# Performance work log

Hardware: AMD Instinct MI355X
Metric: run time of the kernel (lower is better)

The kernel has to match this reference:

```python
import jax, jax.numpy as jnp
import numpy as np

B, S, DM, DE, H, DH, DC, DCq, DR = 4, 2048, 1024, 1024, 16, 64, 128, 128, 32
SCALE = 1.0 / np.sqrt(DH + DR)


def _rope_tables(seq_len, dim, theta=10000.0):
    inv = 1.0 / (theta ** (jnp.arange(0, dim, 2, dtype=jnp.float32) / dim))  # [dim/2]
    t = jnp.arange(seq_len, dtype=jnp.float32)
    ang = t[:, None] * inv[None, :]  # [S, dim/2]
    return jnp.cos(ang), jnp.sin(ang)


def _apply_rope(xq, xk, cos, sin):
    # xq, xk: [B, S, H, DR]; complex rotary on (even, odd) pairs
    def rot(x):
        s = x.shape
        xr = x.reshape(*s[:-1], s[-1] // 2, 2)
        r, i = xr[..., 0], xr[..., 1]
        c = cos[None, :s[1], None, :]
        sn = sin[None, :s[1], None, :]
        out = jnp.stack([r * c - i * sn, r * sn + i * c], axis=-1)
        return out.reshape(s)
    return rot(xq), rot(xk)


def setup_inputs() -> dict:
    key = jax.random.key(0)
    ks = jax.random.split(key, 10)
    def lin(k, din, dout):
        return 0.02 * jax.random.normal(k, (din, dout), jnp.float32)
    inp = {
        "x": jax.random.normal(ks[0], (B, S, DM), jnp.float32),
        "mask": jnp.tril(jnp.ones((S, S), jnp.float32))[None, None],
        "W_dkv": lin(ks[1], DM, DC),  "b_dkv": jnp.zeros((DC,), jnp.float32),
        "W_dq":  lin(ks[2], DM, DCq), "b_dq":  jnp.zeros((DCq,), jnp.float32),
        "W_uk":  lin(ks[3], DC, DE),  "b_uk":  jnp.zeros((DE,), jnp.float32),
        "W_uv":  lin(ks[4], DC, DE),  "b_uv":  jnp.zeros((DE,), jnp.float32),
        "W_uq":  lin(ks[5], DCq, DE), "b_uq":  jnp.zeros((DE,), jnp.float32),
        "W_qr":  lin(ks[6], DCq, DR * H), "b_qr": jnp.zeros((DR * H,), jnp.float32),
        "W_kr":  lin(ks[7], DM, DR),  "b_kr": jnp.zeros((DR,), jnp.float32),
        "W_o":   lin(ks[8], DE, DM),  "b_o":  jnp.zeros((DM,), jnp.float32),
    }
    return inp


def reference(x, mask, W_dkv, b_dkv, W_dq, b_dq, W_uk, b_uk, W_uv, b_uv,
              W_uq, b_uq, W_qr, b_qr, W_kr, b_kr, W_o, b_o):
    bs, seq_len, _ = x.shape
    cos, sin = _rope_tables(2 * S, DR)

    c_q = x @ W_dq + b_dq            # [B,S,DCq]
    c_kv = x @ W_dkv + b_dkv         # [B,S,DC]
    k_r = x @ W_kr + b_kr            # [B,S,DR]

    q_c = (c_q @ W_uq + b_uq).reshape(bs, seq_len, H, DH)
    k_c = (c_kv @ W_uk + b_uk).reshape(bs, seq_len, H, DH)
    v_c = (c_kv @ W_uv + b_uv).reshape(bs, seq_len, H, DH)

    q_r = (c_q @ W_qr + b_qr).reshape(bs, seq_len, H, DR)
    k_r = jnp.broadcast_to(k_r[:, :, None, :], (bs, seq_len, H, DR))
    q_r, k_r = _apply_rope(q_r, k_r, cos, sin)

    q_t = jnp.concatenate([q_c, q_r], axis=-1)  # [B,S,H,DH+DR]
    k_t = jnp.concatenate([k_c, k_r], axis=-1)

    attn = jnp.einsum('bqhd,bkhd->bhqk', q_t, k_t) * SCALE  # [B,H,S,S]
    m = jnp.where(mask == 0, -jnp.inf, mask)  # faithful masked_fill then add
    attn = attn + m
    p = jax.nn.softmax(attn, axis=-1)
    out = jnp.einsum('bhqk,bkhd->bqhd', p, v_c).reshape(bs, seq_len, H * DH)
    return out @ W_o + b_o
```

## Files before the change

### kernel.cpp

```cpp
#include <hip/hip_runtime.h>
#include <cstdint>
#include <cstddef>

#define S_ 2048
#define B_ 4
#define H_ 16
#define ALPHA_Q 0.14724394f

typedef __attribute__((ext_vector_type(8))) __bf16 bf16x8;
typedef __attribute__((ext_vector_type(4))) __bf16 bf16x4;
typedef __attribute__((ext_vector_type(4))) float f32x4;
typedef __attribute__((ext_vector_type(16))) float f32x16;

__device__ __forceinline__ f32x16 mfma32(bf16x8 a, bf16x8 b, f32x16 c) {
  return __builtin_amdgcn_mfma_f32_32x32x16_bf16(a, b, c, 0, 0, 0);
}

__device__ __forceinline__ void gll16(const void* g, void* l) {
  __builtin_amdgcn_global_load_lds(
      (__attribute__((address_space(1))) void*)(uintptr_t)g,
      (__attribute__((address_space(3))) void*)(uint32_t)(uintptr_t)l,
      16, 0, 0);
}

__device__ __forceinline__ int cvtpk(float lo, float hi) {
  int r;
  asm("v_cvt_pk_bf16_f32 %0, %1, %2" : "=v"(r) : "v"(lo), "v"(hi));
  return r;
}

union PAU { int w[4]; bf16x8 v; };

__device__ __forceinline__ bf16x8 packPA(int hi, float a0, float a1, float a2,
                                         float a3, float b0, float b1, float b2,
                                         float b3) {
  const int Ylo = cvtpk(a0, a1);
  const int Yhi = cvtpk(a2, a3);
  const int Xlo = cvtpk(b0, b1);
  const int Xhi = cvtpk(b2, b3);
  const int t0 = __shfl_xor(hi ? Ylo : Xlo, 32);
  const int t1 = __shfl_xor(hi ? Yhi : Xhi, 32);
  PAU u;
  u.w[0] = hi ? t0 : Ylo;
  u.w[1] = hi ? t1 : Yhi;
  u.w[2] = hi ? Xlo : t0;
  u.w[3] = hi ? Xhi : t1;
  return u.v;
}


__global__ __launch_bounds__(256) void mla_cvt_x(const float* __restrict__ x,
                                                 __bf16* __restrict__ xb) {
  const size_t i = ((size_t)blockIdx.x * 256 + threadIdx.x) * 8;
  float4 a = *(const float4*)&x[i];
  float4 b = *(const float4*)&x[i + 4];
  bf16x8 v;
  v[0] = (__bf16)a.x; v[1] = (__bf16)a.y; v[2] = (__bf16)a.z; v[3] = (__bf16)a.w;
  v[4] = (__bf16)b.x; v[5] = (__bf16)b.y; v[6] = (__bf16)b.z; v[7] = (__bf16)b.w;
  *(bf16x8*)&xb[i] = v;
}

__global__ void mla_transpose(const float* __restrict__ W, __bf16* __restrict__ WT,
                              int K, int N) {
  __shared__ float tile[32][33];
  const int n0 = blockIdx.x * 32, k0 = blockIdx.y * 32;
  const int tx = threadIdx.x, ty = threadIdx.y;
#pragma unroll
  for (int i = 0; i < 32; i += 8)
    tile[ty + i][tx] = W[(size_t)(k0 + ty + i) * N + n0 + tx];
  __syncthreads();
#pragma unroll
  for (int i = 0; i < 32; i += 8)
    WT[(size_t)(n0 + ty + i) * K + k0 + tx] = (__bf16)tile[tx][ty + i];
}

__global__ void mla_bias(const float* __restrict__ b_dq, const float* __restrict__ b_dkv,
                         const float* __restrict__ b_kr, const float* __restrict__ b_uq,
                         const float* __restrict__ b_qr, const float* __restrict__ b_uk,
                         const float* __restrict__ b_uv, float* __restrict__ bias_d,
                         float* __restrict__ bias_uq, float* __restrict__ bias_ukv) {
  const int t = blockIdx.x * 256 + threadIdx.x;
  if (t < 384)
    bias_d[t] = (t < 128) ? b_dq[t] : (t < 256) ? b_dkv[t - 128]
               : (t < 288) ? b_kr[t - 256] : 0.f;
  if (t < 1536) bias_uq[t] = (t < 1024) ? b_uq[t] : b_qr[t - 1024];
  if (t < 2048) bias_ukv[t] = (t < 1024) ? b_uk[t] : b_uv[t - 1024];
}

__global__ void mla_rope_tab(float* __restrict__ c, float* __restrict__ sn) {
  const int t = blockIdx.x * 256 + threadIdx.x;
  const int s = t >> 4, i = t & 15;
  const float inv = exp2f(-(float)i * (13.287712379549449f / 16.0f));
  const float ang = (float)s * inv;
  c[t] = cosf(ang);
  sn[t] = sinf(ang);
}

template <int MODE>
__global__ __launch_bounds__(256) void gemm32(
    const __bf16* __restrict__ A, int lda, const __bf16* __restrict__ BT, int ldbt,
    const float* __restrict__ bias, void* __restrict__ C0, void* __restrict__ C1,
    int ldc, int K) {
  const int n0 = blockIdx.x * 128;
  const int m0 = blockIdx.y * 128;
  const int wave = threadIdx.x >> 6, lane = threadIdx.x & 63;
  const int hi = lane >> 5, lq = lane & 31;
  const int wm = (wave >> 1) * 64, wn = (wave & 1) * 64;
  __shared__ __bf16 __attribute__((aligned(16))) ldsA[8 * 128 * 8];
  __shared__ __bf16 __attribute__((aligned(16))) ldsB[8 * 128 * 8];

  const f32x16 fz16 = {0.f, 0.f, 0.f, 0.f, 0.f, 0.f, 0.f, 0.f,
                       0.f, 0.f, 0.f, 0.f, 0.f, 0.f, 0.f, 0.f};
  f32x16 acc00 = fz16, acc01 = fz16, acc10 = fz16, acc11 = fz16;

  for (int k0 = 0; k0 < K; k0 += 64) {
    __syncthreads();
#pragma unroll
    for (int i = 0; i < 8; ++i) {
      const int c = wave * 8 + i;
      if (c < 16) {
        const int sl = c >> 1, half = c & 1;
        gll16(&A[(size_t)(m0 + half * 64 + lane) * lda + k0 + sl * 8],
              &ldsA[(sl * 128 + half * 64) * 8]);
      } else {
        const int cc = c - 16;
        const int sl = cc >> 1, half = cc & 1;
        gll16(&BT[(size_t)(n0 + half * 64 + lane) * ldbt + k0 + sl * 8],
              &ldsB[(sl * 128 + half * 64) * 8]);
      }
    }
    __syncthreads();

#pragma unroll
    for (int ks = 0; ks < 4; ++ks) {
      const int sl = ks * 2 + hi;
      bf16x8 a0 = *(const bf16x8*)&ldsA[(sl * 128 + wm + lq) * 8];
      bf16x8 a1 = *(const bf16x8*)&ldsA[(sl * 128 + wm + 32 + lq) * 8];
      bf16x8 b0 = *(const bf16x8*)&ldsB[(sl * 128 + wn + lq) * 8];
      bf16x8 b1 = *(const bf16x8*)&ldsB[(sl * 128 + wn + 32 + lq) * 8];
      acc00 = mfma32(a0, b0, acc00);
      acc01 = mfma32(a0, b1, acc01);
      acc10 = mfma32(a1, b0, acc10);
      acc11 = mfma32(a1, b1, acc11);
    }
  }

  const f32x16* accs[2][2] = {{&acc00, &acc01}, {&acc10, &acc11}};
#pragma unroll
  for (int ni = 0; ni < 2; ++ni) {
    const int col = n0 + wn + ni * 32 + lq;
    const float bv = bias[col];
#pragma unroll
    for (int mi = 0; mi < 2; ++mi) {
      const f32x16& ac = *accs[mi][ni];
#pragma unroll
      for (int r = 0; r < 16; ++r) {
        const int row = m0 + wm + mi * 32 + (r & 3) + 8 * (r >> 2) + 4 * hi;
        const float v = ac[r] + bv;
        if (MODE == 0) {
          ((__bf16*)C0)[(size_t)row * ldc + col] = (__bf16)v;
        } else if (MODE == 1) {
          ((float*)C0)[(size_t)row * ldc + col] = v;
        } else {
          const int b = row >> 11, s = row & 2047;
          if (col < 1024) {
            const int h = col >> 6, d = col & 63;
            const size_t o = ((size_t)(b * H_ + h) * S_ + s) * 96 + d;
            if (MODE == 2)
              ((__bf16*)C0)[o] = (__bf16)(v * ALPHA_Q);
            else
              ((__bf16*)C0)[o] = (__bf16)v;
          } else {
            if (MODE == 2)
              ((__bf16*)C1)[(size_t)row * 512 + col - 1024] = (__bf16)v;
            else
              ((__bf16*)C1)[(size_t)row * 1024 + col - 1024] = (__bf16)v;
          }
        }
      }
    }
  }
}

__global__ __launch_bounds__(256) void mla_rope_qk(
    const __bf16* __restrict__ qr, const __bf16* __restrict__ cqkvr,
    const float* __restrict__ ropec, const float* __restrict__ ropes,
    __bf16* __restrict__ qt, __bf16* __restrict__ ktb) {
  const int gid = blockIdx.x * 256 + threadIdx.x;
  const int bs = gid >> 8;
  const int h = (gid >> 4) & 15;
  const int i = gid & 15;
  const int b = bs >> 11, s = bs & 2047;
  const float c = ropec[s * 16 + i], sn = ropes[s * 16 + i];
  const size_t o = ((size_t)(b * H_ + h) * S_ + s) * 96 + 64 + 2 * i;
  {
    const float r = (float)qr[(size_t)bs * 512 + h * 32 + 2 * i];
    const float im = (float)qr[(size_t)bs * 512 + h * 32 + 2 * i + 1];
    qt[o] = (__bf16)((r * c - im * sn) * ALPHA_Q);
    qt[o + 1] = (__bf16)((r * sn + im * c) * ALPHA_Q);
  }
  {
    const float r = (float)cqkvr[(size_t)bs * 384 + 256 + 2 * i];
    const float im = (float)cqkvr[(size_t)bs * 384 + 256 + 2 * i + 1];
    ktb[o] = (__bf16)(r * c - im * sn);
    ktb[o + 1] = (__bf16)(r * sn + im * c);
  }
}

__global__ __launch_bounds__(256) void mla_vtrans(const __bf16* __restrict__ vv,
                                                  __bf16* __restrict__ vt) {
  const int s0 = blockIdx.x * 64;
  const int bh = blockIdx.y;
  const int b = bh >> 4, h = bh & 15;
  __shared__ __bf16 __attribute__((aligned(16))) tile[64][72];
  const int t = threadIdx.x;
  {
    const int r = t >> 2, c0 = (t & 3) * 16;
    const size_t src = (size_t)(b * S_ + s0 + r) * 1024 + h * 64 + c0;
    bf16x8 u0 = *(const bf16x8*)&vv[src];
    bf16x8 u1 = *(const bf16x8*)&vv[src + 8];
    *(bf16x8*)&tile[r][c0] = u0;
    *(bf16x8*)&tile[r][c0 + 8] = u1;
  }
  __syncthreads();
  {
    const int d = t >> 2, sc0 = (t & 3) * 16;
    bf16x8 w0, w1;
#pragma unroll
    for (int e = 0; e < 8; ++e) {
      w0[e] = tile[sc0 + e][d];
      w1[e] = tile[sc0 + 8 + e][d];
    }
    const size_t dst = ((size_t)bh * 64 + d) * S_ + s0 + sc0;
    *(bf16x8*)&vt[dst] = w0;
    *(bf16x8*)&vt[dst + 8] = w1;
  }
}

__global__ __launch_bounds__(256, 3) void mla_attn(const __bf16* __restrict__ qt,
                                                   const __bf16* __restrict__ kt,
                                                   const __bf16* __restrict__ vt,
                                                   __bf16* __restrict__ ao) {
  const int qblk = (int)gridDim.x - 1 - blockIdx.x;
  const int bh = blockIdx.y;
  const int wave = threadIdx.x >> 6, lane = threadIdx.x & 63;
  const int hi = lane >> 5, lq = lane & 31;
  const int q0w = qblk * 128 + wave * 32;
  const __bf16* Q = qt + (size_t)bh * S_ * 96;
  const __bf16* Kp = kt + (size_t)bh * S_ * 96;
  const __bf16* Vp = vt + (size_t)bh * 64 * S_;

  __shared__ __bf16 __attribute__((aligned(16))) kbuf[2][12 * 512];
  __shared__ __bf16 __attribute__((aligned(16))) vbuf[2][8 * 512];

  bf16x8 qf[6];
#pragma unroll
  for (int kd = 0; kd < 6; ++kd)
    qf[kd] = *(const bf16x8*)&Q[(size_t)(q0w + lq) * 96 + kd * 16 + hi * 8];

  const f32x16 fz16 = {0.f, 0.f, 0.f, 0.f, 0.f, 0.f, 0.f, 0.f,
                       0.f, 0.f, 0.f, 0.f, 0.f, 0.f, 0.f, 0.f};
  f32x16 o0 = fz16, o1 = fz16;
  float m = -3.0e38f, L = 0.f;

  const int tEnd = (q0w + 31) >> 6;
  const int tMax = qblk * 2 + 1;

  auto stage = [&](int t, int bsel) {
    const int kv0 = t * 64;
#pragma unroll
    for (int i = 0; i < 5; ++i) {
      const int c = wave + 4 * i;
      if (c < 12)
        gll16(&Kp[(size_t)(kv0 + lane) * 96 + c * 8], &kbuf[bsel][c * 512]);
      else
        gll16(&Vp[(size_t)lane * S_ + kv0 + (c - 12) * 8], &vbuf[bsel][(c - 12) * 512]);
    }
  };

  stage(0, 0);
  __syncthreads();

  int bsel = 0;
  for (int t = 0; t <= tMax; ++t) {
    if (t < tMax) stage(t + 1, bsel ^ 1);
    if (t <= tEnd) {
      f32x16 s0 = fz16, s1 = fz16;
#pragma unroll
      for (int kd = 0; kd < 6; ++kd) {
        const int sl = kd * 2 + hi;
        bf16x8 a0 = *(const bf16x8*)&kbuf[bsel][(sl * 64 + lq) * 8];
        bf16x8 a1 = *(const bf16x8*)&kbuf[bsel][(sl * 64 + 32 + lq) * 8];
        s0 = mfma32(a0, qf[kd], s0);
        s1 = mfma32(a1, qf[kd], s1);
      }
      if (t == tEnd) {
        const int qg = q0w + lq;
        const int kvb = t * 64 + 4 * hi;
#pragma unroll
        for (int r = 0; r < 16; ++r) {
          const int crow = (r & 3) + 8 * (r >> 2);
          if (kvb + crow > qg) s0[r] = -3.0e38f;
          if (kvb + 32 + crow > qg) s1[r] = -3.0e38f;
        }
      }
      float tm = s0[0];
#pragma unroll
      for (int r = 1; r < 16; ++r) tm = fmaxf(tm, s0[r]);
#pragma unroll
      for (int r = 0; r < 16; ++r) tm = fmaxf(tm, s1[r]);
      tm = fmaxf(tm, __shfl_xor(tm, 32));
      const float mnew = fmaxf(m, tm);
      float p0[16], p1[16];
      float ps = 0.f;
#pragma unroll
      for (int r = 0; r < 16; ++r) {
        p0[r] = exp2f(s0[r] - mnew);
        p1[r] = exp2f(s1[r] - mnew);
        ps += p0[r] + p1[r];
      }
      ps += __shfl_xor(ps, 32);
      const float sc = exp2f(m - mnew);
      L = L * sc + ps;
      m = mnew;
      o0 *= sc;
      o1 *= sc;
      bf16x8 pa[4];
      pa[0] = packPA(hi, p0[0], p0[1], p0[2], p0[3], p0[4], p0[5], p0[6], p0[7]);
      pa[1] = packPA(hi, p0[8], p0[9], p0[10], p0[11], p0[12], p0[13], p0[14], p0[15]);
      pa[2] = packPA(hi, p1[0], p1[1], p1[2], p1[3], p1[4], p1[5], p1[6], p1[7]);
      pa[3] = packPA(hi, p1[8], p1[9], p1[10], p1[11], p1[12], p1[13], p1[14], p1[15]);
#pragma unroll
      for (int ks = 0; ks < 4; ++ks) {
        const int sl = ks * 2 + hi;
        bf16x8 v0 = *(const bf16x8*)&vbuf[bsel][(sl * 64 + lq) * 8];
        bf16x8 v1 = *(const bf16x8*)&vbuf[bsel][(sl * 64 + 32 + lq) * 8];
        o0 = mfma32(v0, pa[ks], o0);
        o1 = mfma32(v1, pa[ks], o1);
      }
    }
    __syncthreads();
    bsel ^= 1;
  }

  const float invL = 1.0f / L;
  const int bb = bh >> 4, h = bh & 15;
  __bf16* aorow = ao + (size_t)(bb * S_ + q0w + lq) * 1024 + h * 64;
#pragma unroll
  for (int rr = 0; rr < 4; ++rr) {
    bf16x4 w0, w1;
#pragma unroll
    for (int j = 0; j < 4; ++j) {
      w0[j] = (__bf16)(o0[4 * rr + j] * invL);
      w1[j] = (__bf16)(o1[4 * rr + j] * invL);
    }
    *(bf16x4*)&aorow[rr * 8 + 4 * hi] = w0;
    *(bf16x4*)&aorow[32 + rr * 8 + 4 * hi] = w1;
  }
}

extern "C" void kernel_launch(void* const* d_in, const int* in_sizes, int n_in,
                              void* d_out, int out_size, void* d_ws, size_t ws_size,
                              hipStream_t stream) {
  (void)in_sizes; (void)n_in; (void)out_size; (void)ws_size;
  const float* x = (const float*)d_in[0];
  const float* W_dkv = (const float*)d_in[2];
  const float* b_dkv = (const float*)d_in[3];
  const float* W_dq = (const float*)d_in[4];
  const float* b_dq = (const float*)d_in[5];
  const float* W_uk = (const float*)d_in[6];
  const float* b_uk = (const float*)d_in[7];
  const float* W_uv = (const float*)d_in[8];
  const float* b_uv = (const float*)d_in[9];
  const float* W_uq = (const float*)d_in[10];
  const float* b_uq = (const float*)d_in[11];
  const float* W_qr = (const float*)d_in[12];
  const float* b_qr = (const float*)d_in[13];
  const float* W_kr = (const float*)d_in[14];
  const float* b_kr = (const float*)d_in[15];
  const float* W_o = (const float*)d_in[16];
  const float* b_o = (const float*)d_in[17];
  float* out = (float*)d_out;

  char* ws = (char*)d_ws;
  size_t off = 0;
  auto take = [&](size_t nbytes) -> char* {
    char* p = ws + off;
    off += (nbytes + 255) & ~(size_t)255;
    return p;
  };
  __bf16* xb = (__bf16*)take((size_t)8192 * 1024 * 2);
  __bf16* WdT = (__bf16*)take((size_t)384 * 1024 * 2);
  __bf16* WuqT = (__bf16*)take((size_t)1536 * 128 * 2);
  __bf16* WukvT = (__bf16*)take((size_t)2048 * 128 * 2);
  __bf16* WoT = (__bf16*)take((size_t)1024 * 1024 * 2);
  float* bias_d = (float*)take(384 * 4);
  float* bias_uq = (float*)take(1536 * 4);
  float* bias_ukv = (float*)take(2048 * 4);
  float* ropec = (float*)take((size_t)S_ * 16 * 4);
  float* ropes = (float*)take((size_t)S_ * 16 * 4);
  __bf16* cqkvr = (__bf16*)take((size_t)8192 * 384 * 2);
  __bf16* qr = (__bf16*)take((size_t)8192 * 512 * 2);
  __bf16* vv = (__bf16*)take((size_t)8192 * 1024 * 2);
  __bf16* qt = (__bf16*)take((size_t)B_ * H_ * S_ * 96 * 2);
  __bf16* ktb = (__bf16*)take((size_t)B_ * H_ * S_ * 96 * 2);
  __bf16* vt = (__bf16*)take((size_t)B_ * H_ * 64 * S_ * 2);
  __bf16* aout = (__bf16*)take((size_t)8192 * 1024 * 2);

  hipMemsetAsync(WdT + (size_t)288 * 1024, 0, (size_t)96 * 1024 * 2, stream);

  mla_cvt_x<<<4096, 256, 0, stream>>>(x, xb);
  mla_transpose<<<dim3(4, 32), dim3(32, 8), 0, stream>>>(W_dq, WdT, 1024, 128);
  mla_transpose<<<dim3(4, 32), dim3(32, 8), 0, stream>>>(W_dkv, WdT + (size_t)128 * 1024, 1024, 128);
  mla_transpose<<<dim3(1, 32), dim3(32, 8), 0, stream>>>(W_kr, WdT + (size_t)256 * 1024, 1024, 32);
  mla_transpose<<<dim3(32, 4), dim3(32, 8), 0, stream>>>(W_uq, WuqT, 128, 1024);
  mla_transpose<<<dim3(16, 4), dim3(32, 8), 0, stream>>>(W_qr, WuqT + (size_t)1024 * 128, 128, 512);
  mla_transpose<<<dim3(32, 4), dim3(32, 8), 0, stream>>>(W_uk, WukvT, 128, 1024);
  mla_transpose<<<dim3(32, 4), dim3(32, 8), 0, stream>>>(W_uv, WukvT + (size_t)1024 * 128, 128, 1024);
  mla_transpose<<<dim3(32, 32), dim3(32, 8), 0, stream>>>(W_o, WoT, 1024, 1024);
  mla_bias<<<8, 256, 0, stream>>>(b_dq, b_dkv, b_kr, b_uq, b_qr, b_uk, b_uv,
                                  bias_d, bias_uq, bias_ukv);
  mla_rope_tab<<<(S_ * 16) / 256, 256, 0, stream>>>(ropec, ropes);

  gemm32<0><<<dim3(3, 64), 256, 0, stream>>>(xb, 1024, WdT, 1024, bias_d,
                                             cqkvr, nullptr, 384, 1024);
  gemm32<2><<<dim3(12, 64), 256, 0, stream>>>(cqkvr, 384, WuqT, 128, bias_uq,
                                              qt, qr, 0, 128);
  gemm32<3><<<dim3(16, 64), 256, 0, stream>>>(cqkvr + 128, 384, WukvT, 128,
                                              bias_ukv, ktb, vv, 0, 128);

  mla_rope_qk<<<8192, 256, 0, stream>>>(qr, cqkvr, ropec, ropes, qt, ktb);
  mla_vtrans<<<dim3(32, 64), 256, 0, stream>>>(vv, vt);
  mla_attn<<<dim3(16, 64), 256, 0, stream>>>(qt, ktb, vt, aout);

  gemm32<1><<<dim3(8, 64), 256, 0, stream>>>(aout, 1024, WoT, 1024, b_o, out,
                                             nullptr, 1024, 1024);
}
```

Baseline: 412.4 us.

## Merge prep and glue kernels into single launches and use lazy softmax rescale

After: 388.3 us. 1.06x faster.

```diff
diff --git a/kernel.cpp b/kernel.cpp
--- a/kernel.cpp
+++ b/kernel.cpp
@@ -48,52 +48,86 @@
   return u.v;
 }
 
-
-__global__ __launch_bounds__(256) void mla_cvt_x(const float* __restrict__ x,
-                                                 __bf16* __restrict__ xb) {
-  const size_t i = ((size_t)blockIdx.x * 256 + threadIdx.x) * 8;
-  float4 a = *(const float4*)&x[i];
-  float4 b = *(const float4*)&x[i + 4];
-  bf16x8 v;
-  v[0] = (__bf16)a.x; v[1] = (__bf16)a.y; v[2] = (__bf16)a.z; v[3] = (__bf16)a.w;
-  v[4] = (__bf16)b.x; v[5] = (__bf16)b.y; v[6] = (__bf16)b.z; v[7] = (__bf16)b.w;
-  *(bf16x8*)&xb[i] = v;
-}
-
-__global__ void mla_transpose(const float* __restrict__ W, __bf16* __restrict__ WT,
-                              int K, int N) {
+__device__ __forceinline__ float tmax16(const f32x16& v) {
+  float a[8];
+#pragma unroll
+  for (int i = 0; i < 8; ++i) a[i] = fmaxf(v[i], v[i + 8]);
+#pragma unroll
+  for (int s = 4; s > 0; s >>= 1)
+#pragma unroll
+    for (int i = 0; i < s; ++i) a[i] = fmaxf(a[i], a[i + s]);
+  return a[0];
+}
+
+__global__ __launch_bounds__(256) void mla_prep(
+    const float* __restrict__ x, __bf16* __restrict__ xb,
+    const float* __restrict__ W_dq, const float* __restrict__ W_dkv,
+    const float* __restrict__ W_kr, const float* __restrict__ W_uq,
+    const float* __restrict__ W_qr, const float* __restrict__ W_uk,
+    const float* __restrict__ W_uv, const float* __restrict__ W_o,
+    __bf16* __restrict__ WdT, __bf16* __restrict__ WuqT,
+    __bf16* __restrict__ WukvT, __bf16* __restrict__ WoT,
+    const float* __restrict__ b_dq, const float* __restrict__ b_dkv,
+    const float* __restrict__ b_kr, const float* __restrict__ b_uq,
+    const float* __restrict__ b_qr, const float* __restrict__ b_uk,
+    const float* __restrict__ b_uv, float* __restrict__ bias_d,
+    float* __restrict__ bias_uq, float* __restrict__ bias_ukv,
+    float* __restrict__ ropec, float* __restrict__ ropes) {
+  const int id = blockIdx.x;
+  const int t = threadIdx.x;
   __shared__ float tile[32][33];
-  const int n0 = blockIdx.x * 32, k0 = blockIdx.y * 32;
-  const int tx = threadIdx.x, ty = threadIdx.y;
-#pragma unroll
-  for (int i = 0; i < 32; i += 8)
-    tile[ty + i][tx] = W[(size_t)(k0 + ty + i) * N + n0 + tx];
-  __syncthreads();
-#pragma unroll
-  for (int i = 0; i < 32; i += 8)
-    WT[(size_t)(n0 + ty + i) * K + k0 + tx] = (__bf16)tile[tx][ty + i];
-}
-
-__global__ void mla_bias(const float* __restrict__ b_dq, const float* __restrict__ b_dkv,
-                         const float* __restrict__ b_kr, const float* __restrict__ b_uq,
-                         const float* __restrict__ b_qr, const float* __restrict__ b_uk,
-                         const float* __restrict__ b_uv, float* __restrict__ bias_d,
-                         float* __restrict__ bias_uq, float* __restrict__ bias_ukv) {
-  const int t = blockIdx.x * 256 + threadIdx.x;
-  if (t < 384)
-    bias_d[t] = (t < 128) ? b_dq[t] : (t < 256) ? b_dkv[t - 128]
-               : (t < 288) ? b_kr[t - 256] : 0.f;
-  if (t < 1536) bias_uq[t] = (t < 1024) ? b_uq[t] : b_qr[t - 1024];
-  if (t < 2048) bias_ukv[t] = (t < 1024) ? b_uk[t] : b_uv[t - 1024];
-}
-
-__global__ void mla_rope_tab(float* __restrict__ c, float* __restrict__ sn) {
-  const int t = blockIdx.x * 256 + threadIdx.x;
-  const int s = t >> 4, i = t & 15;
-  const float inv = exp2f(-(float)i * (13.287712379549449f / 16.0f));
-  const float ang = (float)s * inv;
-  c[t] = cosf(ang);
-  sn[t] = sinf(ang);
+
+  if (id < 4096) {
+    const size_t i = ((size_t)id * 256 + t) * 8;
+    float4 a = *(const float4*)&x[i];
+    float4 b = *(const float4*)&x[i + 4];
+    bf16x8 v;
+    v[0] = (__bf16)a.x; v[1] = (__bf16)a.y; v[2] = (__bf16)a.z; v[3] = (__bf16)a.w;
+    v[4] = (__bf16)b.x; v[5] = (__bf16)b.y; v[6] = (__bf16)b.z; v[7] = (__bf16)b.w;
+    *(bf16x8*)&xb[i] = v;
+    return;
+  }
+  if (id < 5856) {
+    int rel = id - 4096;
+    const float* W;
+    __bf16* WT;
+    int K, N, nt;
+    if (rel < 128)      { W = W_dq;  WT = WdT;                      K = 1024; N = 128;  nt = 4; }
+    else if (rel < 256) { W = W_dkv; WT = WdT + (size_t)128 * 1024; K = 1024; N = 128;  nt = 4;  rel -= 128; }
+    else if (rel < 288) { W = W_kr;  WT = WdT + (size_t)256 * 1024; K = 1024; N = 32;   nt = 1;  rel -= 256; }
+    else if (rel < 416) { W = W_uq;  WT = WuqT;                     K = 128;  N = 1024; nt = 32; rel -= 288; }
+    else if (rel < 480) { W = W_qr;  WT = WuqT + (size_t)1024 * 128; K = 128; N = 512;  nt = 16; rel -= 416; }
+    else if (rel < 608) { W = W_uk;  WT = WukvT;                    K = 128;  N = 1024; nt = 32; rel -= 480; }
+    else if (rel < 736) { W = W_uv;  WT = WukvT + (size_t)1024 * 128; K = 128; N = 1024; nt = 32; rel -= 608; }
+    else                { W = W_o;   WT = WoT;                      K = 1024; N = 1024; nt = 32; rel -= 736; }
+    const int n0 = (rel % nt) * 32, k0 = (rel / nt) * 32;
+    const int tx = t & 31, ty = t >> 5;
+#pragma unroll
+    for (int i = 0; i < 32; i += 8)
+      tile[ty + i][tx] = W[(size_t)(k0 + ty + i) * N + n0 + tx];
+    __syncthreads();
+#pragma unroll
+    for (int i = 0; i < 32; i += 8)
+      WT[(size_t)(n0 + ty + i) * K + k0 + tx] = (__bf16)tile[tx][ty + i];
+    return;
+  }
+  if (id < 5984) {
+    const int g = (id - 5856) * 256 + t;
+    const int s = g >> 4, i = g & 15;
+    const float inv = exp2f(-(float)i * (13.287712379549449f / 16.0f));
+    const float ang = (float)s * inv;
+    ropec[g] = cosf(ang);
+    ropes[g] = sinf(ang);
+    return;
+  }
+  {
+    const int g = (id - 5984) * 256 + t;
+    if (g < 384)
+      bias_d[g] = (g < 128) ? b_dq[g] : (g < 256) ? b_dkv[g - 128]
+                 : (g < 288) ? b_kr[g - 256] : 0.f;
+    if (g < 1536) bias_uq[g] = (g < 1024) ? b_uq[g] : b_qr[g - 1024];
+    if (g < 2048) bias_ukv[g] = (g < 1024) ? b_uk[g] : b_uv[g - 1024];
+  }
 }
 
 template <int MODE>
@@ -182,38 +216,39 @@
   }
 }
 
-__global__ __launch_bounds__(256) void mla_rope_qk(
+__global__ __launch_bounds__(256) void mla_glue(
     const __bf16* __restrict__ qr, const __bf16* __restrict__ cqkvr,
     const float* __restrict__ ropec, const float* __restrict__ ropes,
-    __bf16* __restrict__ qt, __bf16* __restrict__ ktb) {
-  const int gid = blockIdx.x * 256 + threadIdx.x;
-  const int bs = gid >> 8;
-  const int h = (gid >> 4) & 15;
-  const int i = gid & 15;
-  const int b = bs >> 11, s = bs & 2047;
-  const float c = ropec[s * 16 + i], sn = ropes[s * 16 + i];
-  const size_t o = ((size_t)(b * H_ + h) * S_ + s) * 96 + 64 + 2 * i;
-  {
-    const float r = (float)qr[(size_t)bs * 512 + h * 32 + 2 * i];
-    const float im = (float)qr[(size_t)bs * 512 + h * 32 + 2 * i + 1];
-    qt[o] = (__bf16)((r * c - im * sn) * ALPHA_Q);
-    qt[o + 1] = (__bf16)((r * sn + im * c) * ALPHA_Q);
-  }
-  {
-    const float r = (float)cqkvr[(size_t)bs * 384 + 256 + 2 * i];
-    const float im = (float)cqkvr[(size_t)bs * 384 + 256 + 2 * i + 1];
-    ktb[o] = (__bf16)(r * c - im * sn);
-    ktb[o + 1] = (__bf16)(r * sn + im * c);
-  }
-}
-
-__global__ __launch_bounds__(256) void mla_vtrans(const __bf16* __restrict__ vv,
-                                                  __bf16* __restrict__ vt) {
-  const int s0 = blockIdx.x * 64;
-  const int bh = blockIdx.y;
-  const int b = bh >> 4, h = bh & 15;
+    __bf16* __restrict__ qt, __bf16* __restrict__ ktb,
+    const __bf16* __restrict__ vv, __bf16* __restrict__ vt) {
   __shared__ __bf16 __attribute__((aligned(16))) tile[64][72];
   const int t = threadIdx.x;
+  if (blockIdx.x < 8192) {
+    const int gid = blockIdx.x * 256 + t;
+    const int bs = gid >> 8;
+    const int h = (gid >> 4) & 15;
+    const int i = gid & 15;
+    const int b = bs >> 11, s = bs & 2047;
+    const float c = ropec[s * 16 + i], sn = ropes[s * 16 + i];
+    const size_t o = ((size_t)(b * H_ + h) * S_ + s) * 96 + 64 + 2 * i;
+    {
+      const float r = (float)qr[(size_t)bs * 512 + h * 32 + 2 * i];
+      const float im = (float)qr[(size_t)bs * 512 + h * 32 + 2 * i + 1];
+      qt[o] = (__bf16)((r * c - im * sn) * ALPHA_Q);
+      qt[o + 1] = (__bf16)((r * sn + im * c) * ALPHA_Q);
+    }
+    {
+      const float r = (float)cqkvr[(size_t)bs * 384 + 256 + 2 * i];
+      const float im = (float)cqkvr[(size_t)bs * 384 + 256 + 2 * i + 1];
+      ktb[o] = (__bf16)(r * c - im * sn);
+      ktb[o + 1] = (__bf16)(r * sn + im * c);
+    }
+    return;
+  }
+  const int bid = blockIdx.x - 8192;
+  const int s0 = (bid & 31) * 64;
+  const int bh = bid >> 5;
+  const int b = bh >> 4, h = bh & 15;
   {
     const int r = t >> 2, c0 = (t & 3) * 16;
     const size_t src = (size_t)(b * S_ + s0 + r) * 1024 + h * 64 + c0;
@@ -304,27 +339,32 @@
           if (kvb + 32 + crow > qg) s1[r] = -3.0e38f;
         }
       }
-      float tm = s0[0];
-#pragma unroll
-      for (int r = 1; r < 16; ++r) tm = fmaxf(tm, s0[r]);
-#pragma unroll
-      for (int r = 0; r < 16; ++r) tm = fmaxf(tm, s1[r]);
+      float tm = fmaxf(tmax16(s0), tmax16(s1));
       tm = fmaxf(tm, __shfl_xor(tm, 32));
-      const float mnew = fmaxf(m, tm);
+      if (!__all(tm <= m + 8.0f)) {
+        const float mnew = fmaxf(m, tm);
+        const float sc = exp2f(m - mnew);
+        m = mnew;
+        L *= sc;
+        o0 *= sc;
+        o1 *= sc;
+      }
       float p0[16], p1[16];
-      float ps = 0.f;
 #pragma unroll
       for (int r = 0; r < 16; ++r) {
-        p0[r] = exp2f(s0[r] - mnew);
-        p1[r] = exp2f(s1[r] - mnew);
-        ps += p0[r] + p1[r];
-      }
+        p0[r] = exp2f(s0[r] - m);
+        p1[r] = exp2f(s1[r] - m);
+      }
+      float a[16];
+#pragma unroll
+      for (int r = 0; r < 16; ++r) a[r] = p0[r] + p1[r];
+#pragma unroll
+      for (int s = 8; s > 0; s >>= 1)
+#pragma unroll
+        for (int i = 0; i < s; ++i) a[i] += a[i + s];
+      float ps = a[0];
       ps += __shfl_xor(ps, 32);
-      const float sc = exp2f(m - mnew);
-      L = L * sc + ps;
-      m = mnew;
-      o0 *= sc;
-      o1 *= sc;
+      L += ps;
       bf16x8 pa[4];
       pa[0] = packPA(hi, p0[0], p0[1], p0[2], p0[3], p0[4], p0[5], p0[6], p0[7]);
       pa[1] = packPA(hi, p0[8], p0[9], p0[10], p0[11], p0[12], p0[13], p0[14], p0[15]);
@@ -409,18 +449,10 @@
 
   hipMemsetAsync(WdT + (size_t)288 * 1024, 0, (size_t)96 * 1024 * 2, stream);
 
-  mla_cvt_x<<<4096, 256, 0, stream>>>(x, xb);
-  mla_transpose<<<dim3(4, 32), dim3(32, 8), 0, stream>>>(W_dq, WdT, 1024, 128);
-  mla_transpose<<<dim3(4, 32), dim3(32, 8), 0, stream>>>(W_dkv, WdT + (size_t)128 * 1024, 1024, 128);
-  mla_transpose<<<dim3(1, 32), dim3(32, 8), 0, stream>>>(W_kr, WdT + (size_t)256 * 1024, 1024, 32);
-  mla_transpose<<<dim3(32, 4), dim3(32, 8), 0, stream>>>(W_uq, WuqT, 128, 1024);
-  mla_transpose<<<dim3(16, 4), dim3(32, 8), 0, stream>>>(W_qr, WuqT + (size_t)1024 * 128, 128, 512);
-  mla_transpose<<<dim3(32, 4), dim3(32, 8), 0, stream>>>(W_uk, WukvT, 128, 1024);
-  mla_transpose<<<dim3(32, 4), dim3(32, 8), 0, stream>>>(W_uv, WukvT + (size_t)1024 * 128, 128, 1024);
-  mla_transpose<<<dim3(32, 32), dim3(32, 8), 0, stream>>>(W_o, WoT, 1024, 1024);
-  mla_bias<<<8, 256, 0, stream>>>(b_dq, b_dkv, b_kr, b_uq, b_qr, b_uk, b_uv,
-                                  bias_d, bias_uq, bias_ukv);
-  mla_rope_tab<<<(S_ * 16) / 256, 256, 0, stream>>>(ropec, ropes);
+  mla_prep<<<6000, 256, 0, stream>>>(x, xb, W_dq, W_dkv, W_kr, W_uq, W_qr, W_uk,
+                                     W_uv, W_o, WdT, WuqT, WukvT, WoT, b_dq,
+                                     b_dkv, b_kr, b_uq, b_qr, b_uk, b_uv, bias_d,
+                                     bias_uq, bias_ukv, ropec, ropes);
 
   gemm32<0><<<dim3(3, 64), 256, 0, stream>>>(xb, 1024, WdT, 1024, bias_d,
                                              cqkvr, nullptr, 384, 1024);
@@ -429,8 +461,8 @@
   gemm32<3><<<dim3(16, 64), 256, 0, stream>>>(cqkvr + 128, 384, WukvT, 128,
                                               bias_ukv, ktb, vv, 0, 128);
 
-  mla_rope_qk<<<8192, 256, 0, stream>>>(qr, cqkvr, ropec, ropes, qt, ktb);
-  mla_vtrans<<<dim3(32, 64), 256, 0, stream>>>(vv, vt);
+  mla_glue<<<8192 + 2048, 256, 0, stream>>>(qr, cqkvr, ropec, ropes, qt, ktb, vv, vt);
+
   mla_attn<<<dim3(16, 64), 256, 0, stream>>>(qt, ktb, vt, aout);
 
   gemm32<1><<<dim3(8, 64), 256, 0, stream>>>(aout, 1024, WoT, 1024, b_o, out,
```
